# Kernel optimization log

Hardware: AMD Instinct MI355X
Metric: run time of the kernel (lower is better)

Reference implementation:

```python
import jax, jax.numpy as jnp
import numpy as np

B, T, N, D, F = 32, 12, 1024, 64, 16
KH, DH = 8, 8  # heads, per-head dim; D = KH*DH


def setup_inputs() -> dict:
    key = jax.random.key(0)
    ks = jax.random.split(key, 24)
    def w(i, fi, fo):
        return jax.random.normal(ks[i], (fi, fo), jnp.float32) * (fi ** -0.5)
    adj = jax.random.uniform(ks[0], (N, N), jnp.float32)
    adj = adj / jnp.sum(adj, axis=-1, keepdims=True)  # row-normalized dense adjacency
    z = lambda: jnp.zeros((D,), jnp.float32)
    return dict(
        X=jax.random.normal(ks[1], (B, T, N, D), jnp.float32),
        STE=jax.random.normal(ks[2], (B, T, N, D), jnp.float32),
        adj=adj,
        feat0=jax.random.normal(ks[3], (N, F), jnp.float32),
        feat1=jax.random.normal(ks[4], (N, F), jnp.float32),
        Wq0=w(5, F, D), Wk0=w(6, F, D), Wq1=w(7, F, D), Wk1=w(8, F, D),
        Wgcn=w(9, 4 * D, D), bgcn=z(),
        Wq=w(10, 2 * D, D), bq=z(), Wk=w(11, 2 * D, D), bk=z(), Wv=w(12, 2 * D, D), bv=z(),
        Wx1=w(13, D, D), bx1=z(), Wx2=w(14, D, D), bx2=z(),
        Ws=w(15, D, D), Wt=w(16, D, D), bt=z(),
        Wh1=w(17, D, D), bh1=z(), Wh2=w(18, D, D), bh2=z(),
    )


def reference(X, STE, adj, feat0, feat1, Wq0, Wk0, Wq1, Wk1, Wgcn, bgcn,
              Wq, bq, Wk, bk, Wv, bv, Wx1, bx1, Wx2, bx2,
              Ws, Wt, bt, Wh1, bh1, Wh2, bh2):
    Dm = KH * DH
    # ---- graph conv: static adjacency + feature-driven softmax adjacencies ----
    parts = [X, jnp.einsum('mn,btnd->btmd', adj, X)]
    for feat, Wqf, Wkf in ((feat0, Wq0, Wk0), (feat1, Wq1, Wk1)):
        FEQ = jax.nn.relu(feat @ Wqf)            # [N, D]
        FEK = jax.nn.relu(feat @ Wkf)            # [N, D]
        S = jax.nn.softmax(FEQ @ FEK.T / jnp.sqrt(jnp.float32(Dm)), axis=-1)  # [N, N]
        parts.append(jnp.einsum('mn,btnd->btmd', S, X))
    HS = jax.nn.relu(jnp.concatenate(parts, -1) @ Wgcn + bgcn)  # [B,T,N,D]
    # ---- temporal multi-head self-attention over T ----
    Xc = jnp.concatenate([X, STE], -1)           # [B,T,N,2D]
    b, t, n, _ = Xc.shape
    q = jax.nn.relu(Xc @ Wq + bq).reshape(b, t, n, KH, DH)
    k = jax.nn.relu(Xc @ Wk + bk).reshape(b, t, n, KH, DH)
    v = jax.nn.relu(Xc @ Wv + bv).reshape(b, t, n, KH, DH)
    att = jnp.einsum('btnkd,bsnkd->bknts', q, k) / jnp.sqrt(jnp.float32(DH))
    att = jax.nn.softmax(att, axis=-1)           # [B,K,N,T,T]
    o = jnp.einsum('bknts,bsnkd->btnkd', att, v).reshape(b, t, n, Dm)
    HT = jax.nn.relu(o @ Wx1 + bx1) @ Wx2 + bx2
    # ---- gated fusion ----
    zg = jax.nn.sigmoid(HS @ Ws + HT @ Wt + bt)
    H = zg * HS + (1.0 - zg) * HT
    H = jax.nn.relu(H @ Wh1 + bh1) @ Wh2 + bh2
    return X + H
```

## Files before the change

kernel.cpp:

```cpp
#include <hip/hip_runtime.h>
#include <hip/hip_bf16.h>
#include <hip/hip_fp8.h>
#include <stdint.h>

#define B_ 32
#define T_ 12
#define N_ 1024
#define D_ 64
#define F_ 16
#define KH_ 8
#define BT_ (B_*T_)
#define NROWS_ (BT_*N_)
#define K3_ 3072

typedef unsigned short u16;
typedef unsigned char u8;
struct __align__(8) u16x4 { u16 x, y, z, w; };
struct __align__(16) u16x8 { u16 v[8]; };
typedef __attribute__((ext_vector_type(8))) short short8v;
typedef __attribute__((ext_vector_type(4))) float f32x4;

__device__ __forceinline__ float b2f(u16 u) {
  union { float f; unsigned int i; } c; c.i = ((unsigned int)u) << 16; return c.f;
}
__device__ __forceinline__ u16 f2b(float f) {
  union { float f; unsigned int i; } c; c.f = f;
  unsigned int u = c.i;
  unsigned int r = ((u >> 16) & 1u) + 0x7FFFu;
  return (u16)((u + r) >> 16);
}
__device__ __forceinline__ u8 f2e4(float f) {
  __hip_fp8_e4m3 h(f);
  return (u8)h.__x;
}

__device__ __forceinline__ void gload_lds16(const void* g, void* l) {
  __builtin_amdgcn_global_load_lds(
      (const __attribute__((address_space(1))) unsigned int*)g,
      (__attribute__((address_space(3))) unsigned int*)l, 16, 0, 0);
}

__global__ __launch_bounds__(256) void k_pre(
    const float* __restrict__ feat0, const float* __restrict__ feat1,
    const float* __restrict__ Wq0, const float* __restrict__ Wk0,
    const float* __restrict__ Wq1, const float* __restrict__ Wk1,
    const float* __restrict__ adj,
    const float* __restrict__ Wq, const float* __restrict__ Wk,
    const float* __restrict__ Wv,
    const float* __restrict__ Wx1, const float* __restrict__ Wx2,
    const float* __restrict__ Ws, const float* __restrict__ Wt,
    const float* __restrict__ Wh1, const float* __restrict__ Wh2,
    const float* __restrict__ Wgcn,
    float* __restrict__ fe, float* __restrict__ feKt, u8* __restrict__ Acat8,
    u16* __restrict__ Wqkvt, u16* __restrict__ W1t, u16* __restrict__ W2t,
    u16* __restrict__ Wstt, u16* __restrict__ Wh1t, u16* __restrict__ Wh2t,
    u16* __restrict__ Wgcnt)
{
  int bid = blockIdx.x;
  int t = threadIdx.x;
  if (bid < 1024) {
    int r = bid;
    int m = t >> 6, d = t & 63;
    const float* feat = (m < 2) ? feat0 : feat1;
    const float* W = (m == 0) ? Wq0 : (m == 1) ? Wk0 : (m == 2) ? Wq1 : Wk1;
    float acc = 0.f;
    #pragma unroll
    for (int ff = 0; ff < F_; ++ff) acc += feat[r*F_ + ff] * W[ff*D_ + d];
    float val = fmaxf(acc, 0.f);
    fe[((size_t)m*N_ + r)*D_ + d] = val;
    if (m & 1) {
      int g = m >> 1;
      feKt[((size_t)g*D_ + d)*N_ + r] = val;
    }
  } else if (bid < 2048) {
    int r = bid - 1024;
    for (int c = t; c < N_; c += 256)
      Acat8[(size_t)r*K3_ + c] = f2e4(adj[(size_t)r*N_ + c] * 256.0f);
  } else {
    int g0 = (bid - 2048)*256 + t;
    const int stride = 64*256;
    for (int i = g0; i < 192*128; i += stride) {
      int nn = i >> 7, kk = i & 127;
      const float* W = (nn < 64) ? Wq : (nn < 128) ? Wk : Wv;
      Wqkvt[i] = f2b(W[kk*64 + (nn & 63)]);
    }
    for (int i = g0; i < 64*64; i += stride) {
      int nn = i >> 6, kk = i & 63;
      W1t[i] = f2b(Wx1[kk*64 + nn]);
      W2t[i] = f2b(Wx2[kk*64 + nn]);
      Wh1t[i] = f2b(Wh1[kk*64 + nn]);
      Wh2t[i] = f2b(Wh2[kk*64 + nn]);
    }
    for (int i = g0; i < 64*128; i += stride) {
      int nn = i >> 7, kk = i & 127;
      Wstt[i] = f2b((kk < 64) ? Ws[kk*64 + nn] : Wt[(kk-64)*64 + nn]);
    }
    for (int i = g0; i < 256*64; i += stride) {
      int cc = i >> 6, kk = i & 63;
      Wgcnt[i] = f2b(Wgcn[(size_t)((cc >> 6)*64 + kk)*64 + (cc & 63)]);
    }
  }
}

__global__ __launch_bounds__(256) void k_graph_softmax(const float* __restrict__ fe,
                                                       const float* __restrict__ feKt,
                                                       u8* __restrict__ Acat8) {
  int r = blockIdx.x, g = blockIdx.y;
  const float* FEQ = fe + (size_t)(g*2 + 0)*N_*D_;
  const float* Kt  = feKt + (size_t)g*D_*N_;
  __shared__ float q[D_];
  __shared__ float red[256];
  int tid = threadIdx.x;
  if (tid < D_) q[tid] = FEQ[(size_t)r*D_ + tid];
  __syncthreads();
  float lg[4] = {0.f, 0.f, 0.f, 0.f};
  for (int f = 0; f < D_; ++f) {
    float qf = q[f];
    const float* kt = Kt + (size_t)f*N_;
    #pragma unroll
    for (int j = 0; j < 4; ++j) lg[j] += qf * kt[tid + j*256];
  }
  float mx = -1e30f;
  #pragma unroll
  for (int j = 0; j < 4; ++j) { lg[j] *= 0.125f; mx = fmaxf(mx, lg[j]); }
  red[tid] = mx; __syncthreads();
  for (int s = 128; s > 0; s >>= 1) { if (tid < s) red[tid] = fmaxf(red[tid], red[tid+s]); __syncthreads(); }
  mx = red[0]; __syncthreads();
  float sum = 0.f;
  #pragma unroll
  for (int j = 0; j < 4; ++j) { lg[j] = __expf(lg[j]-mx); sum += lg[j]; }
  red[tid] = sum; __syncthreads();
  for (int s = 128; s > 0; s >>= 1) { if (tid < s) red[tid] += red[tid+s]; __syncthreads(); }
  float inv = 256.0f / red[0];
  #pragma unroll
  for (int j = 0; j < 4; ++j) {
    int c = tid + j*256;
    Acat8[(size_t)r*K3_ + (1+g)*N_ + c] = f2e4(lg[j]*inv);
  }
}

__global__ __launch_bounds__(256) void k_xw_mfma(
    const float* __restrict__ X, const u16* __restrict__ Wgcnt,
    u16* __restrict__ G0, u8* __restrict__ Yt1, u8* __restrict__ Yt2, u8* __restrict__ Yt3)
{
  __shared__ __align__(16) u16 SM[24576];
  u16* Als = SM;
  u16* Bls = SM + 8192;
  u8*  T8  = (u8*)SM;
  u16* Gls = SM;
  int m0 = blockIdx.x * 128;
  int t = threadIdx.x;
  int w = t >> 6, l = t & 63;

  {
    int rsub = l >> 3, pch = l & 7;
    #pragma unroll
    for (int i = 0; i < 8; ++i) {
      int R0 = w*64 + i*8;
      int n = R0 + rsub;
      int q = pch ^ (n & 7);
      gload_lds16(Wgcnt + (size_t)n*64 + q*8, &Bls[R0*64]);
    }
  }
  #pragma unroll
  for (int i = 0; i < 4; ++i) {
    int flat = t + 256*i;
    int row = flat >> 3, c = flat & 7;
    const float* src = X + (size_t)(m0+row)*64 + c*8;
    float4 f0 = *(const float4*)src;
    float4 f1 = *(const float4*)(src + 4);
    u16x8 pk;
    pk.v[0]=f2b(f0.x); pk.v[1]=f2b(f0.y); pk.v[2]=f2b(f0.z); pk.v[3]=f2b(f0.w);
    pk.v[4]=f2b(f1.x); pk.v[5]=f2b(f1.y); pk.v[6]=f2b(f1.z); pk.v[7]=f2b(f1.w);
    int cs = c ^ (row & 7);
    *(u16x8*)&Als[row*64 + cs*8] = pk;
  }
  __syncthreads();

  int wm = w & 1, wn = w >> 1;
  int lr = l & 15, lk = l >> 4;
  f32x4 acc[4][8] = {};
  #pragma unroll
  for (int ks = 0; ks < 2; ++ks) {
    short8v av[4], bv[8];
    #pragma unroll
    for (int fm = 0; fm < 4; ++fm) {
      int r = wm*64 + fm*16 + lr;
      int ch = (ks*4 + lk) ^ (r & 7);
      av[fm] = *(const short8v*)&Als[r*64 + ch*8];
    }
    #pragma unroll
    for (int fn = 0; fn < 8; ++fn) {
      int n = wn*128 + fn*16 + lr;
      int ch = (ks*4 + lk) ^ (n & 7);
      bv[fn] = *(const short8v*)&Bls[n*64 + ch*8];
    }
    #pragma unroll
    for (int fm = 0; fm < 4; ++fm)
      #pragma unroll
      for (int fn = 0; fn < 8; ++fn)
        acc[fm][fn] = __builtin_amdgcn_mfma_f32_16x16x32_bf16(av[fm], bv[fn], acc[fm][fn], 0, 0, 0);
  }
  __syncthreads();

  #pragma unroll
  for (int fm = 0; fm < 4; ++fm) {
    int row0 = wm*64 + fm*16 + lk*4;
    #pragma unroll
    for (int fn = 0; fn < 8; ++fn) {
      int c = wn*128 + fn*16 + lr;
      if (c >= 64) {
        int dp = c - 64;
        unsigned pk = (unsigned)f2e4(acc[fm][fn][0])
                    | ((unsigned)f2e4(acc[fm][fn][1]) << 8)
                    | ((unsigned)f2e4(acc[fm][fn][2]) << 16)
                    | ((unsigned)f2e4(acc[fm][fn][3]) << 24);
        *(unsigned*)&T8[dp*128 + (row0 ^ ((dp & 7) << 3))] = pk;
      }
    }
  }
  __syncthreads();
  {
    int bt = m0 >> 10, nb = m0 & 1023;
    #pragma unroll
    for (int i = 0; i < 12; ++i) {
      int cc = t + 256*i;
      int dp = cc >> 4, nc = cc & 15;
      int n0 = nc*8;
      unsigned long long v8 = *(const unsigned long long*)&T8[dp*128 + (n0 ^ ((dp & 7) << 3))];
      int p = dp >> 6, d = dp & 63;
      u8* Yt = (p == 0) ? Yt1 : (p == 1) ? Yt2 : Yt3;
      *(unsigned long long*)&Yt[((size_t)bt*64 + d)*1024 + nb + n0] = v8;
    }
  }
  __syncthreads();

  if (wn == 0) {
    #pragma unroll
    for (int fm = 0; fm < 4; ++fm) {
      int row0 = wm*64 + fm*16 + lk*4;
      #pragma unroll
      for (int fn = 0; fn < 4; ++fn) {
        int c = fn*16 + lr;
        #pragma unroll
        for (int j = 0; j < 4; ++j) {
          int row = row0 + j;
          Gls[row*64 + (c ^ ((row & 7) << 3))] = f2b(acc[fm][fn][j]);
        }
      }
    }
  }
  __syncthreads();
  #pragma unroll
  for (int i = 0; i < 4; ++i) {
    int cc = t + 256*i;
    int row = cc >> 3, ch = cc & 7;
    u16x8 vv = *(const u16x8*)&Gls[row*64 + ((ch*8) ^ ((row & 7) << 3))];
    *(u16x8*)&G0[(size_t)(m0 + row)*64 + ch*8] = vv;
  }
}

#define BM 128
#define BK3 64
#define NKT3 (K3_/BK3)
__global__ __launch_bounds__(256) void k_spatial_mfma(
    const u8* __restrict__ Acat8,
    const u8* __restrict__ Yt1, const u8* __restrict__ Yt2, const u8* __restrict__ Yt3,
    const float* __restrict__ bgcn,
    u16* __restrict__ HS)
{
  __shared__ __align__(16) u8 SM8[32768];
  int f = blockIdx.x + 8*blockIdx.y;
  int u = f & 7, v = f >> 3;
  int btp = u*24 + (v >> 3);
  int m0  = (v & 7) * BM;
  int bt0 = btp * 2;

  int t = threadIdx.x;
  int w = t >> 6, l = t & 63;
  int rsub = l >> 2, pch = l & 3;

  f32x4 acc[4][4] = {};
  int wm = w >> 1, wn = w & 1;
  int lr = l & 15, lk = l >> 4;

  const u8* aSrc[2];
  size_t bOff[2];
  int R0s[2];
  #pragma unroll
  for (int i = 0; i < 2; ++i) {
    int row = w*32 + i*16 + rsub;
    int q = pch ^ ((row >> 1) & 3);
    aSrc[i] = Acat8 + (size_t)(m0 + row)*K3_ + q*16;
    int bt = bt0 + (row >> 6), d = row & 63;
    bOff[i] = ((size_t)bt*64 + d)*1024 + q*16;
    R0s[i] = w*32 + i*16;
  }

  #pragma unroll
  for (int i = 0; i < 2; ++i) {
    gload_lds16(aSrc[i], &SM8[R0s[i]*64]);
    gload_lds16(Yt1 + bOff[i], &SM8[16384 + R0s[i]*64]);
  }
  __syncthreads();

  int buf = 0;
  for (int kt = 0; kt < NKT3; ++kt) {
    if (kt + 1 < NKT3) {
      int k0 = (kt + 1) * BK3;
      int pl = k0 >> 10, kk = k0 & 1023;
      const u8* Yt = (pl == 0) ? Yt1 : (pl == 1) ? Yt2 : Yt3;
      int bo = (buf ^ 1) * 8192;
      #pragma unroll
      for (int i = 0; i < 2; ++i) {
        gload_lds16(aSrc[i] + k0, &SM8[bo + R0s[i]*64]);
        gload_lds16(Yt + bOff[i] + kk, &SM8[16384 + bo + R0s[i]*64]);
      }
    }
    const u8* A8 = SM8 + buf*8192;
    const u8* B8 = SM8 + 16384 + buf*8192;
    long av[2][4], bv[2][4];
    #pragma unroll
    for (int ks = 0; ks < 2; ++ks) {
      #pragma unroll
      for (int fm = 0; fm < 4; ++fm) {
        int r = wm*64 + fm*16 + lr;
        int g = ks*4 + lk;
        int addr = r*64 + (((g >> 1) ^ ((r >> 1) & 3)) << 4) + ((g & 1) << 3);
        av[ks][fm] = *(const long*)(A8 + addr);
      }
      #pragma unroll
      for (int fn = 0; fn < 4; ++fn) {
        int n = wn*64 + fn*16 + lr;
        int g = ks*4 + lk;
        int addr = n*64 + (((g >> 1) ^ ((n >> 1) & 3)) << 4) + ((g & 1) << 3);
        bv[ks][fn] = *(const long*)(B8 + addr);
      }
    }
    #pragma unroll
    for (int ks = 0; ks < 2; ++ks)
      #pragma unroll
      for (int fm = 0; fm < 4; ++fm)
        #pragma unroll
        for (int fn = 0; fn < 4; ++fn)
          acc[fm][fn] = __builtin_amdgcn_mfma_f32_16x16x32_fp8_fp8(av[ks][fm], bv[ks][fn], acc[fm][fn], 0, 0, 0);
    __syncthreads();
    buf ^= 1;
  }

  u16* Tls = (u16*)SM8;
  #pragma unroll
  for (int fm = 0; fm < 4; ++fm) {
    #pragma unroll
    for (int fn = 0; fn < 4; ++fn) {
      int col = wn*64 + fn*16 + lr;
      int cc = col >> 3, cw = col & 7;
      #pragma unroll
      for (int j = 0; j < 4; ++j) {
        int node = wm*64 + fm*16 + lk*4 + j;
        int sc = cc ^ (node & 7);
        Tls[node*128 + sc*8 + cw] = f2b(acc[fm][fn][j] * 0.00390625f);
      }
    }
  }
  __syncthreads();
  #pragma unroll
  for (int i = 0; i < 8; ++i) {
    int flat = t + 256*i;
    int node = flat >> 4, cc = flat & 15;
    int sc = cc ^ (node & 7);
    u16x8 zv = *(const u16x8*)&Tls[node*128 + sc*8];
    int bt = bt0 + (cc >> 3), d0 = (cc & 7)*8;
    size_t idx = ((size_t)bt*N_ + (m0 + node))*64 + d0;
    u16x8 gv = *(const u16x8*)&HS[idx];
    float4 b0 = *(const float4*)&bgcn[d0];
    float4 b1 = *(const float4*)&bgcn[d0 + 4];
    float bb[8] = { b0.x, b0.y, b0.z, b0.w, b1.x, b1.y, b1.z, b1.w };
    u16x8 ov;
    #pragma unroll
    for (int e = 0; e < 8; ++e) {
      float vv2 = b2f(zv.v[e]) + b2f(gv.v[e]) + bb[e];
      ov.v[e] = f2b(fmaxf(vv2, 0.f));
    }
    *(u16x8*)&HS[idx] = ov;
  }
}

__global__ __launch_bounds__(256) void k_qkv(
    const float* __restrict__ X, const float* __restrict__ STE,
    const u16* __restrict__ Wqkvt,
    const float* __restrict__ bq, const float* __restrict__ bk, const float* __restrict__ bv,
    u16* __restrict__ qb, u16* __restrict__ kb, u16* __restrict__ vb)
{
  __shared__ __align__(16) u16 Als[128*128];
  __shared__ __align__(16) u16 Bls[192*128];
  int m0 = blockIdx.x * 128;
  int t = threadIdx.x;
  int w = t >> 6, l = t & 63;

  {
    int rsub = l >> 4, pch = l & 15;
    #pragma unroll
    for (int i = 0; i < 12; ++i) {
      int R0 = w*48 + i*4;
      int n = R0 + rsub;
      int sq = pch ^ (n & 7);
      gload_lds16(Wqkvt + (size_t)n*128 + sq*8, &Bls[R0*128]);
    }
  }
  #pragma unroll
  for (int i = 0; i < 8; ++i) {
    int flat = t + 256*i;
    int row = flat >> 4, c = flat & 15;
    const float* src = ((c < 8) ? X : STE) + (size_t)(m0+row)*64 + (c & 7)*8;
    float4 f0 = *(const float4*)src;
    float4 f1 = *(const float4*)(src + 4);
    u16x8 pk;
    pk.v[0]=f2b(f0.x); pk.v[1]=f2b(f0.y); pk.v[2]=f2b(f0.z); pk.v[3]=f2b(f0.w);
    pk.v[4]=f2b(f1.x); pk.v[5]=f2b(f1.y); pk.v[6]=f2b(f1.z); pk.v[7]=f2b(f1.w);
    int cs = c ^ (row & 7);
    *(u16x8*)&Als[row*128 + cs*8] = pk;
  }
  __syncthreads();

  int wm = w >> 1, wn = w & 1;
  int lr = l & 15, lk = l >> 4;
  f32x4 acc[4][6] = {};
  #pragma unroll
  for (int ks = 0; ks < 4; ++ks) {
    short8v av[4], bvv[6];
    #pragma unroll
    for (int fm = 0; fm < 4; ++fm) {
      int r = wm*64 + fm*16 + lr;
      int ch = (ks*4 + lk) ^ (r & 7);
      av[fm] = *(const short8v*)&Als[r*128 + ch*8];
    }
    #pragma unroll
    for (int fn = 0; fn < 6; ++fn) {
      int n = wn*96 + fn*16 + lr;
      int ch = (ks*4 + lk) ^ (n & 7);
      bvv[fn] = *(const short8v*)&Bls[n*128 + ch*8];
    }
    #pragma unroll
    for (int fm = 0; fm < 4; ++fm)
      #pragma unroll
      for (int fn = 0; fn < 6; ++fn)
        acc[fm][fn] = __builtin_amdgcn_mfma_f32_16x16x32_bf16(av[fm], bvv[fn], acc[fm][fn], 0, 0, 0);
  }

  #pragma unroll
  for (int fm = 0; fm < 4; ++fm) {
    int rowb = m0 + wm*64 + fm*16 + lk*4;
    #pragma unroll
    for (int fn = 0; fn < 6; ++fn) {
      int col = wn*96 + fn*16 + lr;
      int sel = col >> 6, d = col & 63;
      u16* dst = (sel == 0) ? qb : (sel == 1) ? kb : vb;
      float bias = ((sel == 0) ? bq : (sel == 1) ? bk : bv)[d];
      #pragma unroll
      for (int j = 0; j < 4; ++j) {
        float val = acc[fm][fn][j] + bias;
        dst[(size_t)(rowb + j)*64 + d] = f2b(fmaxf(val, 0.f));
      }
    }
  }
}

__global__ __launch_bounds__(256) void k_attn_ht(
    const u16* __restrict__ qb, const u16* __restrict__ kb, const u16* __restrict__ vb,
    const u16* __restrict__ W1t, const u16* __restrict__ W2t,
    const float* __restrict__ bx1, const float* __restrict__ bx2,
    u16* __restrict__ HT)
{
  __shared__ __align__(16) u16 Ols[48*64];
  __shared__ __align__(16) u16 H1ls[48*64];
  __shared__ __align__(16) u16 W1ls[64*64];
  __shared__ __align__(16) u16 W2ls[64*64];
  int t = threadIdx.x;
  int w = t >> 6, l = t & 63;

  {
    int rsub = l >> 3, pch = l & 7;
    #pragma unroll
    for (int i = 0; i < 2; ++i) {
      int R0 = w*16 + i*8;
      int row = R0 + rsub;
      int sq = pch ^ (row & 7);
      gload_lds16(W1t + (size_t)row*64 + sq*8, &W1ls[R0*64]);
      gload_lds16(W2t + (size_t)row*64 + sq*8, &W2ls[R0*64]);
    }
  }

  int flat = blockIdx.x*4 + w;
  int b = flat >> 10, n = flat & 1023;
  float qv[T_], kv[T_], vv[T_];
  #pragma unroll
  for (int tt = 0; tt < T_; ++tt) {
    size_t idx = ((size_t)(b*T_ + tt)*N_ + n)*64 + l;
    qv[tt] = b2f(qb[idx]); kv[tt] = b2f(kb[idx]); vv[tt] = b2f(vb[idx]);
  }
  #pragma unroll
  for (int tt = 0; tt < T_; ++tt) {
    float sc[T_];
    float mx = -1e30f;
    #pragma unroll
    for (int j = 0; j < T_; ++j) {
      float p = qv[tt]*kv[j];
      p += __shfl_xor(p, 1);
      p += __shfl_xor(p, 2);
      p += __shfl_xor(p, 4);
      sc[j] = p * 0.3535533906f;
      mx = fmaxf(mx, sc[j]);
    }
    float sum = 0.f;
    #pragma unroll
    for (int j = 0; j < T_; ++j) { sc[j] = __expf(sc[j]-mx); sum += sc[j]; }
    float o = 0.f;
    #pragma unroll
    for (int j = 0; j < T_; ++j) o += sc[j]*vv[j];
    int row = w*T_ + tt;
    Ols[row*64 + ((l >> 3) ^ (row & 7))*8 + (l & 7)] = f2b(o / sum);
  }
  __syncthreads();

  int lr = l & 15, lk = l >> 4;
  int col = w*16 + lr;
  f32x4 acc1[3] = {};
  #pragma unroll
  for (int ks = 0; ks < 2; ++ks) {
    short8v av[3], bvv;
    #pragma unroll
    for (int fm = 0; fm < 3; ++fm) {
      int r = fm*16 + lr;
      int ch = (ks*4 + lk) ^ (r & 7);
      av[fm] = *(const short8v*)&Ols[r*64 + ch*8];
    }
    {
      int nn = w*16 + lr;
      int ch = (ks*4 + lk) ^ (nn & 7);
      bvv = *(const short8v*)&W1ls[nn*64 + ch*8];
    }
    #pragma unroll
    for (int fm = 0; fm < 3; ++fm)
      acc1[fm] = __builtin_amdgcn_mfma_f32_16x16x32_bf16(av[fm], bvv, acc1[fm], 0, 0, 0);
  }
  {
    float bias1 = bx1[col];
    #pragma unroll
    for (int fm = 0; fm < 3; ++fm)
      #pragma unroll
      for (int j = 0; j < 4; ++j) {
        int r = fm*16 + lk*4 + j;
        H1ls[r*64 + ((col >> 3) ^ (r & 7))*8 + (col & 7)] = f2b(fmaxf(acc1[fm][j] + bias1, 0.f));
      }
  }
  __syncthreads();

  f32x4 acc2[3] = {};
  #pragma unroll
  for (int ks = 0; ks < 2; ++ks) {
    short8v av[3], bvv;
    #pragma unroll
    for (int fm = 0; fm < 3; ++fm) {
      int r = fm*16 + lr;
      int ch = (ks*4 + lk) ^ (r & 7);
      av[fm] = *(const short8v*)&H1ls[r*64 + ch*8];
    }
    {
      int nn = w*16 + lr;
      int ch = (ks*4 + lk) ^ (nn & 7);
      bvv = *(const short8v*)&W2ls[nn*64 + ch*8];
    }
    #pragma unroll
    for (int fm = 0; fm < 3; ++fm)
      acc2[fm] = __builtin_amdgcn_mfma_f32_16x16x32_bf16(av[fm], bvv, acc2[fm], 0, 0, 0);
  }
  {
    float bias2 = bx2[col];
    #pragma unroll
    for (int fm = 0; fm < 3; ++fm)
      #pragma unroll
      for (int j = 0; j < 4; ++j) {
        int r = fm*16 + lk*4 + j;
        int fp = blockIdx.x*4 + (r / T_);
        int tt = r % T_;
        int b2 = fp >> 10, n2 = fp & 1023;
        HT[((size_t)(b2*T_ + tt)*N_ + n2)*64 + col] = f2b(acc2[fm][j] + bias2);
      }
  }
}

__global__ __launch_bounds__(256) void k_fusion_mfma(
    const float* __restrict__ X,
    const u16* __restrict__ HS, const u16* __restrict__ HT,
    const u16* __restrict__ Wstt, const u16* __restrict__ Wh1t, const u16* __restrict__ Wh2t,
    const float* __restrict__ btb, const float* __restrict__ bh1, const float* __restrict__ bh2,
    float* __restrict__ out)
{
  __shared__ __align__(16) u16 Als[128*128];
  __shared__ __align__(16) u16 Wst[64*128];
  __shared__ __align__(16) u16 W1ls[64*64];
  __shared__ __align__(16) u16 W2ls[64*64];
  __shared__ __align__(16) u16 Hls[128*64];
  int m0 = blockIdx.x * 128;
  int t = threadIdx.x;
  int w = t >> 6, l = t & 63;

  {
    int rsub = l >> 4, pch = l & 15;
    #pragma unroll
    for (int i = 0; i < 8; ++i) {
      int R0 = w*32 + i*4;
      int row = R0 + rsub;
      int q = pch ^ (row & 7);
      const u16* src = (q < 8) ? (HS + (size_t)(m0 + row)*64 + q*8)
                               : (HT + (size_t)(m0 + row)*64 + (q - 8)*8);
      gload_lds16(src, &Als[R0*128]);
    }
    #pragma unroll
    for (int i = 0; i < 4; ++i) {
      int R0 = w*16 + i*4;
      int n = R0 + rsub;
      int q = pch ^ (n & 7);
      gload_lds16(Wstt + (size_t)n*128 + q*8, &Wst[R0*128]);
    }
  }
  {
    int rsub = l >> 3, pch = l & 7;
    #pragma unroll
    for (int i = 0; i < 2; ++i) {
      int R0 = w*16 + i*8;
      int row = R0 + rsub;
      int q = pch ^ (row & 7);
      gload_lds16(Wh1t + (size_t)row*64 + q*8, &W1ls[R0*64]);
      gload_lds16(Wh2t + (size_t)row*64 + q*8, &W2ls[R0*64]);
    }
  }
  __syncthreads();

  int lr = l & 15, lk = l >> 4;
  f32x4 acc1[2][4] = {};
  #pragma unroll
  for (int ks = 0; ks < 4; ++ks) {
    short8v av[2], bvv[4];
    #pragma unroll
    for (int fm = 0; fm < 2; ++fm) {
      int r = w*32 + fm*16 + lr;
      int ch = (ks*4 + lk) ^ (r & 7);
      av[fm] = *(const short8v*)&Als[r*128 + ch*8];
    }
    #pragma unroll
    for (int fn = 0; fn < 4; ++fn) {
      int n = fn*16 + lr;
      int ch = (ks*4 + lk) ^ (n & 7);
      bvv[fn] = *(const short8v*)&Wst[n*128 + ch*8];
    }
    #pragma unroll
    for (int fm = 0; fm < 2; ++fm)
      #pragma unroll
      for (int fn = 0; fn < 4; ++fn)
        acc1[fm][fn] = __builtin_amdgcn_mfma_f32_16x16x32_bf16(av[fm], bvv[fn], acc1[fm][fn], 0, 0, 0);
  }
  #pragma unroll
  for (int fm = 0; fm < 2; ++fm) {
    #pragma unroll
    for (int fn = 0; fn < 4; ++fn) {
      int col = fn*16 + lr;
      float bb = btb[col];
      #pragma unroll
      for (int j = 0; j < 4; ++j) {
        int row = w*32 + fm*16 + lk*4 + j;
        float a_s = acc1[fm][fn][j] + bb;
        float zg = 1.f/(1.f + __expf(-a_s));
        int cs = (col >> 3) ^ (row & 7);
        float hs = b2f(Als[row*128 + cs*8 + (col & 7)]);
        float ht = b2f(Als[row*128 + (cs + 8)*8 + (col & 7)]);
        float H = zg*hs + (1.f - zg)*ht;
        Hls[row*64 + cs*8 + (col & 7)] = f2b(H);
      }
    }
  }
  __syncthreads();

  u16* H2ls = Wst;
  f32x4 acc2[2][4] = {};
  #pragma unroll
  for (int ks = 0; ks < 2; ++ks) {
    short8v av[2], bvv[4];
    #pragma unroll
    for (int fm = 0; fm < 2; ++fm) {
      int r = w*32 + fm*16 + lr;
      int ch = (ks*4 + lk) ^ (r & 7);
      av[fm] = *(const short8v*)&Hls[r*64 + ch*8];
    }
    #pragma unroll
    for (int fn = 0; fn < 4; ++fn) {
      int n = fn*16 + lr;
      int ch = (ks*4 + lk) ^ (n & 7);
      bvv[fn] = *(const short8v*)&W1ls[n*64 + ch*8];
    }
    #pragma unroll
    for (int fm = 0; fm < 2; ++fm)
      #pragma unroll
      for (int fn = 0; fn < 4; ++fn)
        acc2[fm][fn] = __builtin_amdgcn_mfma_f32_16x16x32_bf16(av[fm], bvv[fn], acc2[fm][fn], 0, 0, 0);
  }
  __syncthreads();
  #pragma unroll
  for (int fm = 0; fm < 2; ++fm) {
    #pragma unroll
    for (int fn = 0; fn < 4; ++fn) {
      int col = fn*16 + lr;
      float bias = bh1[col];
      #pragma unroll
      for (int j = 0; j < 4; ++j) {
        int row = w*32 + fm*16 + lk*4 + j;
        float val = acc2[fm][fn][j] + bias;
        int cs = (col >> 3) ^ (row & 7);
        H2ls[row*64 + cs*8 + (col & 7)] = f2b(fmaxf(val, 0.f));
      }
    }
  }
  __syncthreads();

  f32x4 acc3[2][4] = {};
  #pragma unroll
  for (int ks = 0; ks < 2; ++ks) {
    short8v av[2], bvv[4];
    #pragma unroll
    for (int fm = 0; fm < 2; ++fm) {
      int r = w*32 + fm*16 + lr;
      int ch = (ks*4 + lk) ^ (r & 7);
      av[fm] = *(const short8v*)&H2ls[r*64 + ch*8];
    }
    #pragma unroll
    for (int fn = 0; fn < 4; ++fn) {
      int n = fn*16 + lr;
      int ch = (ks*4 + lk) ^ (n & 7);
      bvv[fn] = *(const short8v*)&W2ls[n*64 + ch*8];
    }
    #pragma unroll
    for (int fm = 0; fm < 2; ++fm)
      #pragma unroll
      for (int fn = 0; fn < 4; ++fn)
        acc3[fm][fn] = __builtin_amdgcn_mfma_f32_16x16x32_bf16(av[fm], bvv[fn], acc3[fm][fn], 0, 0, 0);
  }
  #pragma unroll
  for (int fm = 0; fm < 2; ++fm) {
    #pragma unroll
    for (int fn = 0; fn < 4; ++fn) {
      int col = fn*16 + lr;
      float bias = bh2[col];
      #pragma unroll
      for (int j = 0; j < 4; ++j) {
        int row = w*32 + fm*16 + lk*4 + j;
        size_t gi = (size_t)(m0 + row)*64 + col;
        out[gi] = X[gi] + acc3[fm][fn][j] + bias;
      }
    }
  }
}

extern "C" void kernel_launch(void* const* d_in, const int* in_sizes, int n_in,
                              void* d_out, int out_size, void* d_ws, size_t ws_size,
                              hipStream_t stream) {
  const float* X    = (const float*)d_in[0];
  const float* STE  = (const float*)d_in[1];
  const float* adj  = (const float*)d_in[2];
  const float* feat0= (const float*)d_in[3];
  const float* feat1= (const float*)d_in[4];
  const float* Wq0  = (const float*)d_in[5];
  const float* Wk0  = (const float*)d_in[6];
  const float* Wq1  = (const float*)d_in[7];
  const float* Wk1  = (const float*)d_in[8];
  const float* Wgcn = (const float*)d_in[9];
  const float* bgcn = (const float*)d_in[10];
  const float* Wq   = (const float*)d_in[11];
  const float* bq   = (const float*)d_in[12];
  const float* Wk   = (const float*)d_in[13];
  const float* bk   = (const float*)d_in[14];
  const float* Wv   = (const float*)d_in[15];
  const float* bv   = (const float*)d_in[16];
  const float* Wx1  = (const float*)d_in[17];
  const float* bx1  = (const float*)d_in[18];
  const float* Wx2  = (const float*)d_in[19];
  const float* bx2  = (const float*)d_in[20];
  const float* Ws   = (const float*)d_in[21];
  const float* Wt   = (const float*)d_in[22];
  const float* btb  = (const float*)d_in[23];
  const float* Wh1  = (const float*)d_in[24];
  const float* bh1  = (const float*)d_in[25];
  const float* Wh2  = (const float*)d_in[26];
  const float* bh2  = (const float*)d_in[27];
  (void)in_sizes; (void)n_in; (void)out_size;

  const size_t NEEDED = 164626432ull;
  if (ws_size < NEEDED) return;

  char* w = (char*)d_ws;
  float* fe    = (float*)(w);
  u8*    Acat8 = (u8*)(w + 1048576);
  u16*   Wqkvt = (u16*)(w + 7340032);
  u16*   W1t   = (u16*)(w + 7389184);
  u16*   W2t   = (u16*)(w + 7397376);
  u16*   Wstt  = (u16*)(w + 7405568);
  u16*   Wh1t  = (u16*)(w + 7421952);
  u16*   Wh2t  = (u16*)(w + 7430144);
  u16*   Wgcnt = (u16*)(w + 7438336);
  float* feKt  = (float*)(w + 7471104);
  u8*    Yt2   = (u8*)(w + 13631488);
  u8*    Yt3   = (u8*)(w + 63963136);
  u16*   HSb   = (u16*)(w + 114294784);
  u8*    Yt1   = (u8*)d_out;
  u16*   qb    = (u16*)(w + 13631488);
  u16*   kbuf  = (u16*)(w + 63963136);
  u16*   vbuf  = (u16*)d_out;
  u16*   HTb   = qb;

  k_pre<<<2112, 256, 0, stream>>>(feat0, feat1, Wq0, Wk0, Wq1, Wk1, adj,
                                  Wq, Wk, Wv, Wx1, Wx2, Ws, Wt, Wh1, Wh2, Wgcn,
                                  fe, feKt, Acat8, Wqkvt, W1t, W2t, Wstt, Wh1t, Wh2t, Wgcnt);
  k_graph_softmax<<<dim3(N_, 2), 256, 0, stream>>>(fe, feKt, Acat8);
  k_xw_mfma<<<NROWS_/128, 256, 0, stream>>>(X, Wgcnt, HSb, Yt1, Yt2, Yt3);
  k_spatial_mfma<<<dim3(8, BT_/2), 256, 0, stream>>>(Acat8, Yt1, Yt2, Yt3, bgcn, HSb);
  k_qkv<<<NROWS_/128, 256, 0, stream>>>(X, STE, Wqkvt, bq, bk, bv, qb, kbuf, vbuf);
  k_attn_ht<<<(B_*N_)/4, 256, 0, stream>>>(qb, kbuf, vbuf, W1t, W2t, bx1, bx2, HTb);
  k_fusion_mfma<<<NROWS_/128, 256, 0, stream>>>(X, HSb, HTb, Wstt, Wh1t, Wh2t,
                                                btb, bh1, bh2, (float*)d_out);
}
```

Baseline: 547.5 us.

## Compute per-head temporal attention with MFMA instead of scalar shuffle reductions

Stages Q, K and transposed V for each wave's node in LDS. Per head, it computes the 12x12 score matrix with one bf16 MFMA, does the softmax with cross-lane shuffles, packs the probabilities to bf16 and multiplies by V with a second MFMA. This replaces 144 dot products per wave, each built from three shuffles, plus scalar exp/accumulate loops. The cost is a lot of wasted MFMA lanes from zero padding, extra LDS traffic and a block sync, and probabilities rounded to bf16, which lowers accuracy.

Result: faster. 478.6 us (-12.6%).

```diff
diff --git a/kernel.cpp b/kernel.cpp
--- a/kernel.cpp
+++ b/kernel.cpp
@@ -32,6 +32,11 @@
 __device__ __forceinline__ u8 f2e4(float f) {
   __hip_fp8_e4m3 h(f);
   return (u8)h.__x;
+}
+__device__ __forceinline__ unsigned cvt_pk_bf16(float lo, float hi) {
+  unsigned r;
+  asm volatile("v_cvt_pk_bf16_f32 %0, %1, %2" : "=v"(r) : "v"(lo), "v"(hi));
+  return r;
 }
 
 __device__ __forceinline__ void gload_lds16(const void* g, void* l) {
@@ -472,6 +477,9 @@
     const float* __restrict__ bx1, const float* __restrict__ bx2,
     u16* __restrict__ HT)
 {
+  __shared__ __align__(16) u16 QS[4][12*64];
+  __shared__ __align__(16) u16 KS[4][12*64];
+  __shared__ __align__(16) u16 VT[4][64*24];
   __shared__ __align__(16) u16 Ols[48*64];
   __shared__ __align__(16) u16 H1ls[48*64];
   __shared__ __align__(16) u16 W1ls[64*64];
@@ -493,33 +501,73 @@
 
   int flat = blockIdx.x*4 + w;
   int b = flat >> 10, n = flat & 1023;
-  float qv[T_], kv[T_], vv[T_];
-  #pragma unroll
-  for (int tt = 0; tt < T_; ++tt) {
-    size_t idx = ((size_t)(b*T_ + tt)*N_ + n)*64 + l;
-    qv[tt] = b2f(qb[idx]); kv[tt] = b2f(kb[idx]); vv[tt] = b2f(vb[idx]);
-  }
-  #pragma unroll
-  for (int tt = 0; tt < T_; ++tt) {
-    float sc[T_];
-    float mx = -1e30f;
-    #pragma unroll
-    for (int j = 0; j < T_; ++j) {
-      float p = qv[tt]*kv[j];
-      p += __shfl_xor(p, 1);
-      p += __shfl_xor(p, 2);
-      p += __shfl_xor(p, 4);
-      sc[j] = p * 0.3535533906f;
-      mx = fmaxf(mx, sc[j]);
-    }
-    float sum = 0.f;
-    #pragma unroll
-    for (int j = 0; j < T_; ++j) { sc[j] = __expf(sc[j]-mx); sum += sc[j]; }
-    float o = 0.f;
-    #pragma unroll
-    for (int j = 0; j < T_; ++j) o += sc[j]*vv[j];
-    int row = w*T_ + tt;
-    Ols[row*64 + ((l >> 3) ^ (row & 7))*8 + (l & 7)] = f2b(o / sum);
+  {
+    int ch = l >> 3, e = l & 7;
+    #pragma unroll
+    for (int tt = 0; tt < T_; ++tt) {
+      size_t idx = ((size_t)(b*T_ + tt)*N_ + n)*64 + l;
+      u16 qv = qb[idx], kv = kb[idx], vv = vb[idx];
+      int sl = (ch ^ (tt & 7))*8 + e;
+      QS[w][tt*64 + sl] = qv;
+      KS[w][tt*64 + sl] = kv;
+      VT[w][l*24 + tt] = vv;
+    }
+    #pragma unroll
+    for (int tt = T_; tt < 16; ++tt) VT[w][l*24 + tt] = 0;
+  }
+  __syncthreads();
+
+  int g = l >> 4;
+  int sr = l & 15;
+  short8v z8 = {0,0,0,0,0,0,0,0};
+  float scale = 0.3535533906f;
+
+  for (int h = 0; h < KH_; ++h) {
+    short8v kf = *(const short8v*)&KS[w][sr*64 + ((h ^ (sr & 7)) << 3)];
+    short8v qf = *(const short8v*)&QS[w][sr*64 + ((h ^ (sr & 7)) << 3)];
+    short8v avk = (l < 16) ? kf : z8;
+    short8v bvq = (l < 16) ? qf : z8;
+    f32x4 zc = {0.f, 0.f, 0.f, 0.f};
+    f32x4 S = __builtin_amdgcn_mfma_f32_16x16x32_bf16(avk, bvq, zc, 0, 0, 0);
+    float sc0 = S[0]*scale, sc1 = S[1]*scale, sc2 = S[2]*scale, sc3 = S[3]*scale;
+    bool gv = (g < 3);
+    float mown = gv ? fmaxf(fmaxf(sc0, sc1), fmaxf(sc2, sc3)) : -1e30f;
+    float m1 = fmaxf(mown, __shfl_xor(mown, 16));
+    float m2 = fmaxf(m1, __shfl_xor(m1, 48));
+    float e0 = gv ? __expf(sc0 - m2) : 0.f;
+    float e1 = gv ? __expf(sc1 - m2) : 0.f;
+    float e2 = gv ? __expf(sc2 - m2) : 0.f;
+    float e3 = gv ? __expf(sc3 - m2) : 0.f;
+    float ss = e0 + e1 + e2 + e3;
+    float s1 = ss + __shfl_xor(ss, 16);
+    float s2 = s1 + __shfl_xor(s1, 48);
+    float rn = 1.0f / s2;
+    float p0 = e0*rn, p1 = e1*rn, p2 = e2*rn, p3 = e3*rn;
+    float pa0 = __shfl_xor(p0, 16), pa1 = __shfl_xor(p1, 16),
+          pa2 = __shfl_xor(p2, 16), pa3 = __shfl_xor(p3, 16);
+    float pb0 = __shfl_xor(p0, 48), pb1 = __shfl_xor(p1, 48),
+          pb2 = __shfl_xor(p2, 48), pb3 = __shfl_xor(p3, 48);
+    float v0, v1, v2, v3, v4, v5, v6, v7;
+    if (g == 0)      { v0=p0;  v1=p1;  v2=p2;  v3=p3;  v4=pa0; v5=pa1; v6=pa2; v7=pa3; }
+    else if (g == 1) { v0=pb0; v1=pb1; v2=pb2; v3=pb3; v4=0;   v5=0;   v6=0;   v7=0;   }
+    else             { v0=0; v1=0; v2=0; v3=0; v4=0; v5=0; v6=0; v7=0; }
+    union { unsigned u[4]; short8v s; } pk;
+    pk.u[0] = cvt_pk_bf16(v0, v1);
+    pk.u[1] = cvt_pk_bf16(v2, v3);
+    pk.u[2] = cvt_pk_bf16(v4, v5);
+    pk.u[3] = cvt_pk_bf16(v6, v7);
+    int vrow = h*8 + (l & 7);
+    short8v vf = *(const short8v*)&VT[w][vrow*24 + ((l >> 4) & 1)*8];
+    short8v av2 = (g < 2) ? vf : z8;
+    f32x4 O = __builtin_amdgcn_mfma_f32_16x16x32_bf16(av2, pk.s, zc, 0, 0, 0);
+    if (g < 2 && sr < T_) {
+      int r = w*T_ + sr;
+      unsigned lo = cvt_pk_bf16(O[0], O[1]);
+      unsigned hi = cvt_pk_bf16(O[2], O[3]);
+      unsigned off = (unsigned)(r*64 + ((h ^ (r & 7)) << 3) + g*4);
+      uint2 pr; pr.x = lo; pr.y = hi;
+      *(uint2*)&Ols[off] = pr;
+    }
   }
   __syncthreads();
 
```
